# Optimization experiments

Measured on AMD Instinct MI355X. Metric: run time of the kernel, lower is better.

Reference implementation:

```python
import jax, jax.numpy as jnp
import numpy as np

EPS = 1e-5

def _ln(x):
    # non-affine LayerNorm over last dim
    m = jnp.mean(x, axis=-1, keepdims=True)
    v = jnp.var(x, axis=-1, keepdims=True)
    return (x - m) / jnp.sqrt(v + EPS)

def setup_inputs() -> dict:
    key = jax.random.key(0)
    ks = jax.random.split(key, 6)
    B, D_in, H = 16384, 512, 512
    bound_i = 1.0 / np.sqrt(D_in)
    bound_h = 1.0 / np.sqrt(H)
    x = jax.random.normal(ks[0], (B, D_in), dtype=jnp.float32)
    hx = jax.random.normal(ks[1], (B, H), dtype=jnp.float32)
    W_i2h = jax.random.uniform(ks[2], (3 * H, D_in), minval=-bound_i, maxval=bound_i, dtype=jnp.float32)
    b_i2h = jax.random.uniform(ks[3], (3 * H,), minval=-bound_i, maxval=bound_i, dtype=jnp.float32)
    W_h2h = jax.random.uniform(ks[4], (3 * H, H), minval=-bound_h, maxval=bound_h, dtype=jnp.float32)
    b_h2h = jax.random.uniform(ks[5], (3 * H,), minval=-bound_h, maxval=bound_h, dtype=jnp.float32)
    return {"x": x, "hx": hx, "W_i2h": W_i2h, "b_i2h": b_i2h, "W_h2h": W_h2h, "b_h2h": b_h2h}

def reference(x, hx, W_i2h, b_i2h, W_h2h, b_h2h):
    H = hx.shape[-1]
    xt = x @ W_i2h.T + b_i2h        # [B, 3H]
    ht = hx @ W_h2h.T + b_h2h       # [B, 3H]
    x_new = xt[:, 2 * H:]
    h_new = ht[:, 2 * H:]
    gates = jax.nn.sigmoid(_ln(xt[:, : 2 * H]) + _ln(ht[:, : 2 * H]))
    r_t = gates[:, :H]
    z_t = gates[:, H:]
    n_t = jnp.tanh(_ln(x_new) + r_t * _ln(h_new))
    h_t = z_t * hx + (1.0 - z_t) * n_t
    return h_t
```

## Files before the change

### kernel.cpp

```cpp
#include <hip/hip_runtime.h>

#define M_ROWS 16384
#define N_COLS 1536
#define K_DIM  512
#define H_DIM  512

typedef __attribute__((ext_vector_type(8))) short short8;
typedef __attribute__((ext_vector_type(4))) float f32x4;

__device__ __forceinline__ unsigned short f2bf(float f) {
  unsigned u = __float_as_uint(f);
  u += 0x7fffu + ((u >> 16) & 1u);
  return (unsigned short)(u >> 16);
}
__device__ __forceinline__ float bf2f(unsigned short h) {
  return __uint_as_float(((unsigned)h) << 16);
}

__device__ __forceinline__ void gload_lds16(const void* g, void* l) {
  __builtin_amdgcn_global_load_lds((const __attribute__((address_space(1))) void*)g,
                                   (__attribute__((address_space(3))) void*)l,
                                   16, 0, 0);
}

__global__ __launch_bounds__(256) void cvt_all(
    const float* __restrict__ x, const float* __restrict__ hx,
    const float* __restrict__ Wi, const float* __restrict__ Wh,
    unsigned short* __restrict__ xb, unsigned short* __restrict__ hxb,
    unsigned short* __restrict__ Wib, unsigned short* __restrict__ Whb) {
  int i = blockIdx.x * blockDim.x + threadIdx.x;
  const float* s; unsigned short* d; int off;
  if (i < 2097152)      { s = x;  d = xb;  off = i; }
  else if (i < 4194304) { s = hx; d = hxb; off = i - 2097152; }
  else if (i < 4390912) { s = Wi; d = Wib; off = i - 4194304; }
  else                  { s = Wh; d = Whb; off = i - 4390912; }
  float4 f = ((const float4*)s)[off];
  ushort4 u;
  u.x = f2bf(f.x); u.y = f2bf(f.y); u.z = f2bf(f.z); u.w = f2bf(f.w);
  ((ushort4*)d)[off] = u;
}

__global__ __launch_bounds__(256) void gemm_bf16(
    const unsigned short* __restrict__ xb, const unsigned short* __restrict__ hxb,
    const unsigned short* __restrict__ Wib, const unsigned short* __restrict__ Whb,
    const float* __restrict__ b_i2h, const float* __restrict__ b_h2h,
    unsigned short* __restrict__ xt, unsigned short* __restrict__ ht) {
  const int mat = blockIdx.z;
  const unsigned short* A  = mat ? hxb : xb;
  const unsigned short* Bw = mat ? Whb : Wib;
  const float* bias        = mat ? b_h2h : b_i2h;
  unsigned short* outp     = mat ? ht : xt;

  const int m0 = blockIdx.x * 128;
  const int n0 = blockIdx.y * 128;

  __shared__ short lds[2 * 128 * 64];
  short* ldsA = lds;
  short* ldsB = lds + 128 * 64;

  const int t = threadIdx.x;
  const int w = t >> 6, lane = t & 63;
  const int w_row = w >> 1, w_col = w & 1;
  const int lane15 = lane & 15, quad = lane >> 4;

  f32x4 acc[4][4];
#pragma unroll
  for (int i = 0; i < 4; ++i)
#pragma unroll
    for (int j = 0; j < 4; ++j) acc[i][j] = (f32x4){0.f, 0.f, 0.f, 0.f};

  const int srow = lane >> 3;
  const int scol = ((lane & 7) ^ srow) * 8;

  for (int k0 = 0; k0 < K_DIM; k0 += 64) {
#pragma unroll
    for (int q = 0; q < 4; ++q) {
      const int base_row = w * 32 + q * 8;
      gload_lds16(A  + (size_t)(m0 + base_row + srow) * K_DIM + k0 + scol,
                  &ldsA[base_row * 64]);
      gload_lds16(Bw + (size_t)(n0 + base_row + srow) * K_DIM + k0 + scol,
                  &ldsB[base_row * 64]);
    }
    __syncthreads();
#pragma unroll
    for (int kk = 0; kk < 2; ++kk) {
      short8 af[4], bf[4];
      const int l7 = lane15 & 7;
#pragma unroll
      for (int i = 0; i < 4; ++i)
        af[i] = *(const short8*)&ldsA[(w_row * 64 + i * 16 + lane15) * 64 +
                                      (((kk * 4 + quad) ^ l7) * 8)];
#pragma unroll
      for (int j = 0; j < 4; ++j)
        bf[j] = *(const short8*)&ldsB[(w_col * 64 + j * 16 + lane15) * 64 +
                                      (((kk * 4 + quad) ^ l7) * 8)];
#pragma unroll
      for (int i = 0; i < 4; ++i)
#pragma unroll
        for (int j = 0; j < 4; ++j)
          acc[i][j] = __builtin_amdgcn_mfma_f32_16x16x32_bf16(af[i], bf[j], acc[i][j], 0, 0, 0);
    }
    __syncthreads();
  }

  float bj[4];
#pragma unroll
  for (int j = 0; j < 4; ++j) bj[j] = bias[n0 + w_col * 64 + j * 16 + lane15];

#pragma unroll
  for (int i = 0; i < 4; ++i) {
#pragma unroll
    for (int r = 0; r < 4; ++r) {
      const int rowl = w_row * 64 + i * 16 + quad * 4 + r;
      ushort4 pk;
      pk.x = f2bf(acc[i][0][r] + bj[0]);
      pk.y = f2bf(acc[i][1][r] + bj[1]);
      pk.z = f2bf(acc[i][2][r] + bj[2]);
      pk.w = f2bf(acc[i][3][r] + bj[3]);
      *(ushort4*)(outp + (size_t)(m0 + rowl) * N_COLS + n0 + w_col * 64 + lane15 * 4) = pk;
    }
  }
}

__global__ __launch_bounds__(256) void finalize_kernel(
    const unsigned short* __restrict__ xt, const unsigned short* __restrict__ ht,
    const float* __restrict__ hx, float* __restrict__ out) {
  const int w = threadIdx.x >> 6, lane = threadIdx.x & 63;
  const int b = blockIdx.x * 4 + w;
  const size_t rb = (size_t)b * N_COLS;
  const int la = lane & 7, lb = lane >> 3;

  short8 sxr = *(const short8*)&xt[rb + 8 * lane];
  short8 sxz = *(const short8*)&xt[rb + 512 + 8 * lane];
  short8 sxn = *(const short8*)&xt[rb + 1024 + 8 * lane];
  short8 shr = *(const short8*)&ht[rb + 8 * lane];
  short8 shz = *(const short8*)&ht[rb + 512 + 8 * lane];
  short8 shn = *(const short8*)&ht[rb + 1024 + 8 * lane];

  float vxr[8], vxz[8], vxn[8], vhr[8], vhz[8], vhn[8];
#pragma unroll
  for (int k = 0; k < 8; ++k) {
    vxr[k] = bf2f((unsigned short)sxr[k]);
    vxz[k] = bf2f((unsigned short)sxz[k]);
    vxn[k] = bf2f((unsigned short)sxn[k]);
    vhr[k] = bf2f((unsigned short)shr[k]);
    vhz[k] = bf2f((unsigned short)shz[k]);
    vhn[k] = bf2f((unsigned short)shn[k]);
  }

  float pr[8] = {0.f, 0.f, 0.f, 0.f, 0.f, 0.f, 0.f, 0.f};
#pragma unroll
  for (int k = 0; k < 8; ++k) {
    pr[0] += vxr[k] + vxz[k];
    pr[1] += vxr[k] * vxr[k] + vxz[k] * vxz[k];
    pr[2] += vxn[k];
    pr[3] += vxn[k] * vxn[k];
    pr[4] += vhr[k] + vhz[k];
    pr[5] += vhr[k] * vhr[k] + vhz[k] * vhz[k];
    pr[6] += vhn[k];
    pr[7] += vhn[k] * vhn[k];
  }
#pragma unroll
  for (int msk = 1; msk < 64; msk <<= 1)
#pragma unroll
    for (int k = 0; k < 8; ++k) pr[k] += __shfl_xor(pr[k], msk);

  const float inv2H = 1.f / 1024.f, invH = 1.f / 512.f;
  const float mx0 = pr[0] * inv2H;
  const float ix0 = rsqrtf(pr[1] * inv2H - mx0 * mx0 + 1e-5f);
  const float mx1 = pr[2] * invH;
  const float ix1 = rsqrtf(pr[3] * invH - mx1 * mx1 + 1e-5f);
  const float mh0 = pr[4] * inv2H;
  const float ih0 = rsqrtf(pr[5] * inv2H - mh0 * mh0 + 1e-5f);
  const float mh1 = pr[6] * invH;
  const float ih1 = rsqrtf(pr[7] * invH - mh1 * mh1 + 1e-5f);

  auto calc = [&](float xrv, float xzv, float xnv, float hrv, float hzv,
                  float hnv, float hxs) -> float {
    float ar = (xrv - mx0) * ix0 + (hrv - mh0) * ih0;
    float az = (xzv - mx0) * ix0 + (hzv - mh0) * ih0;
    float r = 1.f / (1.f + __expf(-ar));
    float z = 1.f / (1.f + __expf(-az));
    float arg = (xnv - mx1) * ix1 + r * ((hnv - mh1) * ih1);
    float e2 = __expf(2.f * arg);
    float nn = (e2 - 1.f) / (e2 + 1.f);
    return z * hxs + (1.f - z) * nn;
  };

  const float* hxrow = hx + (size_t)b * H_DIM;
  float* orow = out + (size_t)b * H_DIM;
#pragma unroll
  for (int j = 0; j < 4; ++j) {
    const int col = lb * 64 + j * 16 + 2 * la;
    float2 hxv = *(const float2*)&hxrow[col];
    float2 res;
    res.x = calc(vxr[j], vxz[j], vxn[j], vhr[j], vhz[j], vhn[j], hxv.x);
    res.y = calc(vxr[j + 4], vxz[j + 4], vxn[j + 4], vhr[j + 4], vhz[j + 4],
                 vhn[j + 4], hxv.y);
    *(float2*)&orow[col] = res;
  }
}

extern "C" void kernel_launch(void* const* d_in, const int* in_sizes, int n_in,
                              void* d_out, int out_size, void* d_ws, size_t ws_size,
                              hipStream_t stream) {
  const float* x  = (const float*)d_in[0];
  const float* hx = (const float*)d_in[1];
  const float* Wi = (const float*)d_in[2];
  const float* bi = (const float*)d_in[3];
  const float* Wh = (const float*)d_in[4];
  const float* bh = (const float*)d_in[5];
  float* out = (float*)d_out;

  char* ws = (char*)d_ws;
  unsigned short* xb  = (unsigned short*)(ws);
  unsigned short* hxb = (unsigned short*)(ws + 16777216);
  unsigned short* Wib = (unsigned short*)(ws + 33554432);
  unsigned short* Whb = (unsigned short*)(ws + 35127296);
  unsigned short* xt  = (unsigned short*)(ws + 36700160);
  unsigned short* ht  = (unsigned short*)(ws + 87031808);

  cvt_all<<<17920, 256, 0, stream>>>(x, hx, Wi, Wh, xb, hxb, Wib, Whb);

  gemm_bf16<<<dim3(M_ROWS / 128, N_COLS / 128, 2), 256, 0, stream>>>(
      xb, hxb, Wib, Whb, bi, bh, xt, ht);

  finalize_kernel<<<M_ROWS / 4, 256, 0, stream>>>(xt, ht, hx, out);
}
```

Baseline: 206.8 us.

## Switch GEMM to 32x32x16 MFMA and read bf16 hx in finalize

Replaces the 4x4 grid of 16x16x32 MFMA tiles per wave with a 2x2 grid of 32x32x16 MFMA tiles. This changes the LDS fragment loads, the accumulator layout and the bias/store epilogue, which now writes ushort2 pairs with an interleaved column permutation. It also adds a min-blocks hint to the launch bounds. The finalize kernel now reads the bf16 copy of hx instead of fp32 and remaps its output columns to float4 stores. That cuts memory traffic but blends with bf16-rounded hx, which loses precision, and the new permuted column layout has to stay consistent between the GEMM store and the finalize load.

```diff
diff --git a/kernel.cpp b/kernel.cpp
--- a/kernel.cpp
+++ b/kernel.cpp
@@ -6,7 +6,7 @@
 #define H_DIM  512
 
 typedef __attribute__((ext_vector_type(8))) short short8;
-typedef __attribute__((ext_vector_type(4))) float f32x4;
+typedef __attribute__((ext_vector_type(16))) float f32x16;
 
 __device__ __forceinline__ unsigned short f2bf(float f) {
   unsigned u = __float_as_uint(f);
@@ -40,7 +40,7 @@
   ((ushort4*)d)[off] = u;
 }
 
-__global__ __launch_bounds__(256) void gemm_bf16(
+__global__ __launch_bounds__(256, 4) void gemm_bf16(
     const unsigned short* __restrict__ xb, const unsigned short* __restrict__ hxb,
     const unsigned short* __restrict__ Wib, const unsigned short* __restrict__ Whb,
     const float* __restrict__ b_i2h, const float* __restrict__ b_h2h,
@@ -61,13 +61,15 @@
   const int t = threadIdx.x;
   const int w = t >> 6, lane = t & 63;
   const int w_row = w >> 1, w_col = w & 1;
-  const int lane15 = lane & 15, quad = lane >> 4;
-
-  f32x4 acc[4][4];
-#pragma unroll
-  for (int i = 0; i < 4; ++i)
-#pragma unroll
-    for (int j = 0; j < 4; ++j) acc[i][j] = (f32x4){0.f, 0.f, 0.f, 0.f};
+  const int l31 = lane & 31, h = lane >> 5;
+
+  f32x16 acc[2][2];
+#pragma unroll
+  for (int i = 0; i < 2; ++i)
+#pragma unroll
+    for (int j = 0; j < 2; ++j)
+#pragma unroll
+      for (int r = 0; r < 16; ++r) acc[i][j][r] = 0.f;
 
   const int srow = lane >> 3;
   const int scol = ((lane & 7) ^ srow) * 8;
@@ -83,52 +85,56 @@
     }
     __syncthreads();
 #pragma unroll
-    for (int kk = 0; kk < 2; ++kk) {
-      short8 af[4], bf[4];
-      const int l7 = lane15 & 7;
-#pragma unroll
-      for (int i = 0; i < 4; ++i)
-        af[i] = *(const short8*)&ldsA[(w_row * 64 + i * 16 + lane15) * 64 +
-                                      (((kk * 4 + quad) ^ l7) * 8)];
-#pragma unroll
-      for (int j = 0; j < 4; ++j)
-        bf[j] = *(const short8*)&ldsB[(w_col * 64 + j * 16 + lane15) * 64 +
-                                      (((kk * 4 + quad) ^ l7) * 8)];
-#pragma unroll
-      for (int i = 0; i < 4; ++i)
-#pragma unroll
-        for (int j = 0; j < 4; ++j)
-          acc[i][j] = __builtin_amdgcn_mfma_f32_16x16x32_bf16(af[i], bf[j], acc[i][j], 0, 0, 0);
+    for (int kk = 0; kk < 4; ++kk) {
+      const int chunk = ((kk * 2 + h) ^ (l31 & 7)) * 8;
+      short8 af[2], bf[2];
+#pragma unroll
+      for (int i = 0; i < 2; ++i)
+        af[i] = *(const short8*)&ldsA[(w_row * 64 + i * 32 + l31) * 64 + chunk];
+#pragma unroll
+      for (int j = 0; j < 2; ++j)
+        bf[j] = *(const short8*)&ldsB[(w_col * 64 + j * 32 + l31) * 64 + chunk];
+#pragma unroll
+      for (int i = 0; i < 2; ++i)
+#pragma unroll
+        for (int j = 0; j < 2; ++j)
+          acc[i][j] = __builtin_amdgcn_mfma_f32_32x32x16_bf16(af[i], bf[j], acc[i][j], 0, 0, 0);
     }
     __syncthreads();
   }
 
-  float bj[4];
-#pragma unroll
-  for (int j = 0; j < 4; ++j) bj[j] = bias[n0 + w_col * 64 + j * 16 + lane15];
-
-#pragma unroll
-  for (int i = 0; i < 4; ++i) {
-#pragma unroll
-    for (int r = 0; r < 4; ++r) {
-      const int rowl = w_row * 64 + i * 16 + quad * 4 + r;
-      ushort4 pk;
-      pk.x = f2bf(acc[i][0][r] + bj[0]);
-      pk.y = f2bf(acc[i][1][r] + bj[1]);
-      pk.z = f2bf(acc[i][2][r] + bj[2]);
-      pk.w = f2bf(acc[i][3][r] + bj[3]);
-      *(ushort4*)(outp + (size_t)(m0 + rowl) * N_COLS + n0 + w_col * 64 + lane15 * 4) = pk;
+  float bj0[2], bj1[2];
+#pragma unroll
+  for (int j = 0; j < 2; ++j) {
+    bj0[j] = bias[n0 + w_col * 64 + 0 * 32 + l31] * 0.f;
+  }
+  const float biasj0 = bias[n0 + w_col * 64 + l31];
+  const float biasj1 = bias[n0 + w_col * 64 + 32 + l31];
+
+#pragma unroll
+  for (int i = 0; i < 2; ++i) {
+#pragma unroll
+    for (int g = 0; g < 4; ++g) {
+#pragma unroll
+      for (int d = 0; d < 4; ++d) {
+        const int reg = g * 4 + d;
+        const int row = d + 8 * g + 4 * h;
+        ushort2 pk;
+        pk.x = f2bf(acc[i][0][reg] + biasj0);
+        pk.y = f2bf(acc[i][1][reg] + biasj1);
+        *(ushort2*)(outp + (size_t)(m0 + w_row * 64 + i * 32 + row) * N_COLS +
+                    n0 + w_col * 64 + 2 * l31) = pk;
+      }
     }
   }
 }
 
 __global__ __launch_bounds__(256) void finalize_kernel(
     const unsigned short* __restrict__ xt, const unsigned short* __restrict__ ht,
-    const float* __restrict__ hx, float* __restrict__ out) {
+    const unsigned short* __restrict__ hxb, float* __restrict__ out) {
   const int w = threadIdx.x >> 6, lane = threadIdx.x & 63;
   const int b = blockIdx.x * 4 + w;
   const size_t rb = (size_t)b * N_COLS;
-  const int la = lane & 7, lb = lane >> 3;
 
   short8 sxr = *(const short8*)&xt[rb + 8 * lane];
   short8 sxz = *(const short8*)&xt[rb + 512 + 8 * lane];
@@ -187,18 +193,27 @@
     return z * hxs + (1.f - z) * nn;
   };
 
-  const float* hxrow = hx + (size_t)b * H_DIM;
+  const int base4 = 64 * (lane >> 3) + 4 * (lane & 7);
+  const unsigned short* hxrow = hxb + (size_t)b * H_DIM;
   float* orow = out + (size_t)b * H_DIM;
-#pragma unroll
-  for (int j = 0; j < 4; ++j) {
-    const int col = lb * 64 + j * 16 + 2 * la;
-    float2 hxv = *(const float2*)&hxrow[col];
-    float2 res;
-    res.x = calc(vxr[j], vxz[j], vxn[j], vhr[j], vhz[j], vhn[j], hxv.x);
-    res.y = calc(vxr[j + 4], vxz[j + 4], vxn[j + 4], vhr[j + 4], vhz[j + 4],
-                 vhn[j + 4], hxv.y);
-    *(float2*)&orow[col] = res;
-  }
+
+  ushort4 hx0u = *(const ushort4*)&hxrow[base4];
+  ushort4 hx1u = *(const ushort4*)&hxrow[base4 + 32];
+  float hx0[4] = {bf2f(hx0u.x), bf2f(hx0u.y), bf2f(hx0u.z), bf2f(hx0u.w)};
+  float hx1[4] = {bf2f(hx1u.x), bf2f(hx1u.y), bf2f(hx1u.z), bf2f(hx1u.w)};
+
+  float4 r0, r1;
+  float* r0p = (float*)&r0;
+  float* r1p = (float*)&r1;
+#pragma unroll
+  for (int k = 0; k < 4; ++k) {
+    r0p[k] = calc(vxr[2 * k], vxz[2 * k], vxn[2 * k],
+                  vhr[2 * k], vhz[2 * k], vhn[2 * k], hx0[k]);
+    r1p[k] = calc(vxr[2 * k + 1], vxz[2 * k + 1], vxn[2 * k + 1],
+                  vhr[2 * k + 1], vhz[2 * k + 1], vhn[2 * k + 1], hx1[k]);
+  }
+  *(float4*)&orow[base4] = r0;
+  *(float4*)&orow[base4 + 32] = r1;
 }
 
 extern "C" void kernel_launch(void* const* d_in, const int* in_sizes, int n_in,
@@ -225,5 +240,5 @@
   gemm_bf16<<<dim3(M_ROWS / 128, N_COLS / 128, 2), 256, 0, stream>>>(
       xb, hxb, Wib, Whb, bi, bh, xt, ht);
 
-  finalize_kernel<<<M_ROWS / 4, 256, 0, stream>>>(xt, ht, hx, out);
-}
+  finalize_kernel<<<M_ROWS / 4, 256, 0, stream>>>(xt, ht, hxb, out);
+}
```

After: 202.5 us. -2.1%, faster.
